# Kernel optimization log

Hardware: AMD Instinct MI355X
Metric: run time of the kernel (lower is better)

The kernel has to match this reference:

```python
import jax, jax.numpy as jnp
import numpy as np

ALPHAS = (0.1, 0.3, 0.6)
WEIGHTS = (0.5, 0.3, 0.2)
HUBER_MARGIN = 1.0
B, S = 2048, 8192


def setup_inputs() -> dict:
    key = jax.random.key(0)
    k1, k2 = jax.random.split(key)
    pred = jax.random.normal(k1, (B, S), dtype=jnp.float32)
    target = jax.random.normal(k2, (B, S), dtype=jnp.float32)
    return {"pred": pred, "target": target}


def _ema(x, alpha):
    # x: [B, S]; ema[0] = x[0]; ema[i] = alpha*x[i] + (1-alpha)*ema[i-1]
    x0 = x[:, 0]
    def step(carry, xi):
        nc = alpha * xi + (1.0 - alpha) * carry
        return nc, nc
    _, ys = jax.lax.scan(step, x0, x[:, 1:].T)  # ys: [S-1, B]
    return jnp.concatenate([x0[:, None], ys.T], axis=1)  # [B, S]


def _huber_loss(pred_delta, target_delta):
    dir_agreement = pred_delta * target_delta
    step_err = jnp.abs(pred_delta - target_delta)
    quad = jnp.square(jnp.maximum(HUBER_MARGIN - dir_agreement, 0.0)) / (2.0 * HUBER_MARGIN)
    return jnp.where(dir_agreement < 0, step_err, quad).mean(axis=1)  # [B]


def reference(pred, target):
    loss = jnp.zeros((pred.shape[0],), dtype=pred.dtype)
    for alpha, weight in zip(ALPHAS, WEIGHTS):
        pe = _ema(pred, alpha)
        te = _ema(target, alpha)
        pd = pe[:, 1:] - pe[:, :-1]
        td = te[:, 1:] - te[:, :-1]
        loss = loss + weight * _huber_loss(pd, td)
    return loss.mean()  # reduction='mean'
```

## Files before the change

### kernel.cpp

```cpp
#include <hip/hip_runtime.h>

#define B_ROWS 2048
#define S_LEN 8192
#define PER_LANE 32
#define TILE_ELEMS (64 * PER_LANE)
#define NTILES (S_LEN / TILE_ELEMS)
#define WPB 4
#define NBLOCKS (B_ROWS / WPB)

constexpr double cpowi(double b, int e) { double r = 1.0; for (int i = 0; i < e; ++i) r *= b; return r; }
constexpr float tof(double x) { return (x < 1.2e-38 && x > -1.2e-38) ? 0.0f : (float)x; }

#define A0f 0.1f
#define A1f 0.3f
#define A2f 0.6f

constexpr float D0_1 = tof(cpowi(0.9, 32)),  D0_2 = tof(cpowi(0.9, 64)),  D0_4 = tof(cpowi(0.9, 128));
constexpr float D0_8 = tof(cpowi(0.9, 256)), D0_16 = tof(cpowi(0.9, 512)), D0_32 = tof(cpowi(0.9, 1024));
constexpr float D1_1 = tof(cpowi(0.7, 32)),  D1_2 = tof(cpowi(0.7, 64)),  D1_4 = tof(cpowi(0.7, 128));
constexpr float D1_8 = tof(cpowi(0.7, 256)), D1_16 = tof(cpowi(0.7, 512)), D1_32 = tof(cpowi(0.7, 1024));
constexpr float D2_1 = tof(cpowi(0.4, 32)),  D2_2 = tof(cpowi(0.4, 64)),  D2_4 = tof(cpowi(0.4, 128));
constexpr float D2_8 = tof(cpowi(0.4, 256)), D2_16 = tof(cpowi(0.4, 512)), D2_32 = tof(cpowi(0.4, 1024));

__device__ __forceinline__ float ema_scan(float v, int lane,
                                          float d1, float d2, float d4,
                                          float d8, float d16, float d32) {
    float u;
    u = __shfl_up(v, 1);  v += (lane >= 1  ? d1  : 0.0f) * u;
    u = __shfl_up(v, 2);  v += (lane >= 2  ? d2  : 0.0f) * u;
    u = __shfl_up(v, 4);  v += (lane >= 4  ? d4  : 0.0f) * u;
    u = __shfl_up(v, 8);  v += (lane >= 8  ? d8  : 0.0f) * u;
    u = __shfl_up(v, 16); v += (lane >= 16 ? d16 : 0.0f) * u;
    u = __shfl_up(v, 32); v += (lane >= 32 ? d32 : 0.0f) * u;
    return v;
}

__device__ __forceinline__ float huber(float pd, float td) {
    float dir = pd * td;
    float se  = fabsf(pd - td);
    float mm  = fmaxf(1.0f - dir, 0.0f);
    float q   = 0.5f * mm * mm;
    return dir < 0.0f ? se : q;
}

__global__ void __launch_bounds__(256) msl_main(const float* __restrict__ pred,
                                                const float* __restrict__ targ,
                                                float* __restrict__ partial) {
    const int lane = threadIdx.x & 63;
    const int wave = threadIdx.x >> 6;
    const int row  = blockIdx.x * WPB + wave;
    const float* __restrict__ prow = pred + (size_t)row * S_LEN;
    const float* __restrict__ trow = targ + (size_t)row * S_LEN;

    float sp0 = 0.f, sp1 = 0.f, sp2 = 0.f, st0 = 0.f, st1 = 0.f, st2 = 0.f;
    float acc0 = 0.f, acc1 = 0.f, acc2 = 0.f;

    for (int tile = 0; tile < NTILES; ++tile) {
        const int base = tile * TILE_ELEMS + lane * PER_LANE;
        float xp[PER_LANE], xt[PER_LANE];
        const float4* p4 = reinterpret_cast<const float4*>(prow + base);
        const float4* t4 = reinterpret_cast<const float4*>(trow + base);
#pragma unroll
        for (int j = 0; j < PER_LANE / 4; ++j) {
            float4 a = p4[j];
            float4 b = t4[j];
            xp[4 * j + 0] = a.x; xp[4 * j + 1] = a.y; xp[4 * j + 2] = a.z; xp[4 * j + 3] = a.w;
            xt[4 * j + 0] = b.x; xt[4 * j + 1] = b.y; xt[4 * j + 2] = b.z; xt[4 * j + 3] = b.w;
        }

        const bool first = (tile == 0);
        const bool lz    = (lane == 0);

        float Lp0 = lz ? (first ? xp[0] : sp0) : 0.0f;
        float Lp1 = lz ? (first ? xp[0] : sp1) : 0.0f;
        float Lp2 = lz ? (first ? xp[0] : sp2) : 0.0f;
        float Lt0 = lz ? (first ? xt[0] : st0) : 0.0f;
        float Lt1 = lz ? (first ? xt[0] : st1) : 0.0f;
        float Lt2 = lz ? (first ? xt[0] : st2) : 0.0f;
#pragma unroll
        for (int j = 0; j < PER_LANE; ++j) {
            Lp0 += A0f * (xp[j] - Lp0);
            Lp1 += A1f * (xp[j] - Lp1);
            Lp2 += A2f * (xp[j] - Lp2);
            Lt0 += A0f * (xt[j] - Lt0);
            Lt1 += A1f * (xt[j] - Lt1);
            Lt2 += A2f * (xt[j] - Lt2);
        }

        float vp0 = ema_scan(Lp0, lane, D0_1, D0_2, D0_4, D0_8, D0_16, D0_32);
        float vp1 = ema_scan(Lp1, lane, D1_1, D1_2, D1_4, D1_8, D1_16, D1_32);
        float vp2 = ema_scan(Lp2, lane, D2_1, D2_2, D2_4, D2_8, D2_16, D2_32);
        float vt0 = ema_scan(Lt0, lane, D0_1, D0_2, D0_4, D0_8, D0_16, D0_32);
        float vt1 = ema_scan(Lt1, lane, D1_1, D1_2, D1_4, D1_8, D1_16, D1_32);
        float vt2 = ema_scan(Lt2, lane, D2_1, D2_2, D2_4, D2_8, D2_16, D2_32);

        float cp0 = __shfl_up(vp0, 1), cp1 = __shfl_up(vp1, 1), cp2 = __shfl_up(vp2, 1);
        float ct0 = __shfl_up(vt0, 1), ct1 = __shfl_up(vt1, 1), ct2 = __shfl_up(vt2, 1);

        float yp0 = lz ? (first ? xp[0] : sp0) : cp0;
        float yp1 = lz ? (first ? xp[0] : sp1) : cp1;
        float yp2 = lz ? (first ? xp[0] : sp2) : cp2;
        float yt0 = lz ? (first ? xt[0] : st0) : ct0;
        float yt1 = lz ? (first ? xt[0] : st1) : ct1;
        float yt2 = lz ? (first ? xt[0] : st2) : ct2;

        sp0 = __shfl(vp0, 63); sp1 = __shfl(vp1, 63); sp2 = __shfl(vp2, 63);
        st0 = __shfl(vt0, 63); st1 = __shfl(vt1, 63); st2 = __shfl(vt2, 63);

        const float skip = (first && lz) ? 0.0f : 1.0f;
#pragma unroll
        for (int j = 0; j < PER_LANE; ++j) {
            float pd0 = A0f * (xp[j] - yp0); yp0 += pd0;
            float td0 = A0f * (xt[j] - yt0); yt0 += td0;
            float pd1 = A1f * (xp[j] - yp1); yp1 += pd1;
            float td1 = A1f * (xt[j] - yt1); yt1 += td1;
            float pd2 = A2f * (xp[j] - yp2); yp2 += pd2;
            float td2 = A2f * (xt[j] - yt2); yt2 += td2;

            float h0 = huber(pd0, td0);
            float h1 = huber(pd1, td1);
            float h2 = huber(pd2, td2);
            if (j == 0) { h0 *= skip; h1 *= skip; h2 *= skip; }
            acc0 += h0; acc1 += h1; acc2 += h2;
        }
    }

    float wacc = 0.5f * acc0 + 0.3f * acc1 + 0.2f * acc2;
#pragma unroll
    for (int o = 32; o > 0; o >>= 1) wacc += __shfl_down(wacc, o);

    __shared__ float sred[WPB];
    if (lane == 0) sred[wave] = wacc;
    __syncthreads();
    if (threadIdx.x == 0)
        partial[blockIdx.x] = sred[0] + sred[1] + sred[2] + sred[3];
}

__global__ void __launch_bounds__(256) msl_reduce(const float* __restrict__ partial,
                                                  float* __restrict__ out) {
    const int tid = threadIdx.x;
    float v = partial[tid] + partial[tid + 256];
#pragma unroll
    for (int o = 32; o > 0; o >>= 1) v += __shfl_down(v, o);
    __shared__ float s[4];
    if ((tid & 63) == 0) s[tid >> 6] = v;
    __syncthreads();
    if (tid == 0)
        out[0] = (s[0] + s[1] + s[2] + s[3]) *
                 (float)(1.0 / ((double)(S_LEN - 1) * (double)B_ROWS));
}

extern "C" void kernel_launch(void* const* d_in, const int* in_sizes, int n_in,
                              void* d_out, int out_size, void* d_ws, size_t ws_size,
                              hipStream_t stream) {
    const float* pred = (const float*)d_in[0];
    const float* targ = (const float*)d_in[1];
    float* out = (float*)d_out;
    float* partial = (float*)d_ws;

    msl_main<<<NBLOCKS, 256, 0, stream>>>(pred, targ, partial);
    msl_reduce<<<1, 256, 0, stream>>>(partial, out);
}
```

Before: 157.4 us.

## Split rows into warm-started segments and replace reduce kernel with atomics

Each row is split into 8 segments of 1024 outputs, each handled by its own wave, which recomputes a 256-element warm-up window so the EMA state decays enough to be ignored. This gives 8x more waves and removes the serial tile loop per row. The second reduction kernel is replaced by a memset and a per-block atomicAdd. The warm-up truncation is an approximation: with alpha 0.1 the state decays by 0.9^256 (about 2e-12), which is below float precision. It costs about 25% extra loads and compute, and the atomic sum makes the result order nondeterministic.

```diff
diff --git a/kernel.cpp b/kernel.cpp
--- a/kernel.cpp
+++ b/kernel.cpp
@@ -2,36 +2,38 @@
 
 #define B_ROWS 2048
 #define S_LEN 8192
-#define PER_LANE 32
-#define TILE_ELEMS (64 * PER_LANE)
-#define NTILES (S_LEN / TILE_ELEMS)
+#define SEG_OUT 1024
+#define WARM 256
+#define EXT (SEG_OUT + WARM)
+#define PER_LANE (EXT / 64)
+#define NSEG (S_LEN / SEG_OUT)
 #define WPB 4
-#define NBLOCKS (B_ROWS / WPB)
+#define NBLOCKS (B_ROWS * NSEG / WPB)
 
 constexpr double cpowi(double b, int e) { double r = 1.0; for (int i = 0; i < e; ++i) r *= b; return r; }
-constexpr float tof(double x) { return (x < 1.2e-38 && x > -1.2e-38) ? 0.0f : (float)x; }
+constexpr float trim(double x) { return (x < 1e-12 && x > -1e-12) ? 0.0f : (float)x; }
 
 #define A0f 0.1f
 #define A1f 0.3f
 #define A2f 0.6f
 
-constexpr float D0_1 = tof(cpowi(0.9, 32)),  D0_2 = tof(cpowi(0.9, 64)),  D0_4 = tof(cpowi(0.9, 128));
-constexpr float D0_8 = tof(cpowi(0.9, 256)), D0_16 = tof(cpowi(0.9, 512)), D0_32 = tof(cpowi(0.9, 1024));
-constexpr float D1_1 = tof(cpowi(0.7, 32)),  D1_2 = tof(cpowi(0.7, 64)),  D1_4 = tof(cpowi(0.7, 128));
-constexpr float D1_8 = tof(cpowi(0.7, 256)), D1_16 = tof(cpowi(0.7, 512)), D1_32 = tof(cpowi(0.7, 1024));
-constexpr float D2_1 = tof(cpowi(0.4, 32)),  D2_2 = tof(cpowi(0.4, 64)),  D2_4 = tof(cpowi(0.4, 128));
-constexpr float D2_8 = tof(cpowi(0.4, 256)), D2_16 = tof(cpowi(0.4, 512)), D2_32 = tof(cpowi(0.4, 1024));
+constexpr float D0_1 = trim(cpowi(0.9, 20)),  D0_2 = trim(cpowi(0.9, 40)),  D0_4 = trim(cpowi(0.9, 80));
+constexpr float D0_8 = trim(cpowi(0.9, 160)), D0_16 = trim(cpowi(0.9, 320)), D0_32 = trim(cpowi(0.9, 640));
+constexpr float D1_1 = trim(cpowi(0.7, 20)),  D1_2 = trim(cpowi(0.7, 40)),  D1_4 = trim(cpowi(0.7, 80));
+constexpr float D1_8 = trim(cpowi(0.7, 160)), D1_16 = trim(cpowi(0.7, 320)), D1_32 = trim(cpowi(0.7, 640));
+constexpr float D2_1 = trim(cpowi(0.4, 20)),  D2_2 = trim(cpowi(0.4, 40)),  D2_4 = trim(cpowi(0.4, 80));
+constexpr float D2_8 = trim(cpowi(0.4, 160)), D2_16 = trim(cpowi(0.4, 320)), D2_32 = trim(cpowi(0.4, 640));
 
 __device__ __forceinline__ float ema_scan(float v, int lane,
                                           float d1, float d2, float d4,
                                           float d8, float d16, float d32) {
     float u;
-    u = __shfl_up(v, 1);  v += (lane >= 1  ? d1  : 0.0f) * u;
-    u = __shfl_up(v, 2);  v += (lane >= 2  ? d2  : 0.0f) * u;
-    u = __shfl_up(v, 4);  v += (lane >= 4  ? d4  : 0.0f) * u;
-    u = __shfl_up(v, 8);  v += (lane >= 8  ? d8  : 0.0f) * u;
-    u = __shfl_up(v, 16); v += (lane >= 16 ? d16 : 0.0f) * u;
-    u = __shfl_up(v, 32); v += (lane >= 32 ? d32 : 0.0f) * u;
+    if (d1 != 0.0f) { u = __shfl_up(v, 1);  v += (lane >= 1  ? d1  : 0.0f) * u; }
+    if (d2 != 0.0f) { u = __shfl_up(v, 2);  v += (lane >= 2  ? d2  : 0.0f) * u; }
+    if (d4 != 0.0f) { u = __shfl_up(v, 4);  v += (lane >= 4  ? d4  : 0.0f) * u; }
+    if (d8 != 0.0f) { u = __shfl_up(v, 8);  v += (lane >= 8  ? d8  : 0.0f) * u; }
+    if (d16 != 0.0f) { u = __shfl_up(v, 16); v += (lane >= 16 ? d16 : 0.0f) * u; }
+    if (d32 != 0.0f) { u = __shfl_up(v, 32); v += (lane >= 32 ? d32 : 0.0f) * u; }
     return v;
 }
 
@@ -45,84 +47,80 @@
 
 __global__ void __launch_bounds__(256) msl_main(const float* __restrict__ pred,
                                                 const float* __restrict__ targ,
-                                                float* __restrict__ partial) {
+                                                float* __restrict__ out) {
     const int lane = threadIdx.x & 63;
     const int wave = threadIdx.x >> 6;
-    const int row  = blockIdx.x * WPB + wave;
-    const float* __restrict__ prow = pred + (size_t)row * S_LEN;
-    const float* __restrict__ trow = targ + (size_t)row * S_LEN;
+    const int g    = blockIdx.x * WPB + wave;
+    const int row  = g >> 3;
+    const int seg  = g & 7;
+    const bool s0  = (seg == 0);
+    const bool lz  = (lane == 0);
 
-    float sp0 = 0.f, sp1 = 0.f, sp2 = 0.f, st0 = 0.f, st1 = 0.f, st2 = 0.f;
+    const int ext_base = s0 ? 0 : seg * SEG_OUT - WARM;
+    const int lo = s0 ? 1 : WARM;
+    const int hi = s0 ? SEG_OUT : EXT;
+
+    const float* __restrict__ prow = pred + (size_t)row * S_LEN + ext_base + lane * PER_LANE;
+    const float* __restrict__ trow = targ + (size_t)row * S_LEN + ext_base + lane * PER_LANE;
+
+    float xp[PER_LANE], xt[PER_LANE];
+    const float4* p4 = reinterpret_cast<const float4*>(prow);
+    const float4* t4 = reinterpret_cast<const float4*>(trow);
+#pragma unroll
+    for (int j = 0; j < PER_LANE / 4; ++j) {
+        float4 a = p4[j];
+        float4 b = t4[j];
+        xp[4 * j + 0] = a.x; xp[4 * j + 1] = a.y; xp[4 * j + 2] = a.z; xp[4 * j + 3] = a.w;
+        xt[4 * j + 0] = b.x; xt[4 * j + 1] = b.y; xt[4 * j + 2] = b.z; xt[4 * j + 3] = b.w;
+    }
+
+    const float ip = (lz && s0) ? xp[0] : 0.0f;
+    const float it = (lz && s0) ? xt[0] : 0.0f;
+    float Lp0 = ip, Lp1 = ip, Lp2 = ip;
+    float Lt0 = it, Lt1 = it, Lt2 = it;
+#pragma unroll
+    for (int j = 0; j < PER_LANE; ++j) {
+        Lp0 += A0f * (xp[j] - Lp0);
+        Lp1 += A1f * (xp[j] - Lp1);
+        Lp2 += A2f * (xp[j] - Lp2);
+        Lt0 += A0f * (xt[j] - Lt0);
+        Lt1 += A1f * (xt[j] - Lt1);
+        Lt2 += A2f * (xt[j] - Lt2);
+    }
+
+    float vp0 = ema_scan(Lp0, lane, D0_1, D0_2, D0_4, D0_8, D0_16, D0_32);
+    float vp1 = ema_scan(Lp1, lane, D1_1, D1_2, D1_4, D1_8, D1_16, D1_32);
+    float vp2 = ema_scan(Lp2, lane, D2_1, D2_2, D2_4, D2_8, D2_16, D2_32);
+    float vt0 = ema_scan(Lt0, lane, D0_1, D0_2, D0_4, D0_8, D0_16, D0_32);
+    float vt1 = ema_scan(Lt1, lane, D1_1, D1_2, D1_4, D1_8, D1_16, D1_32);
+    float vt2 = ema_scan(Lt2, lane, D2_1, D2_2, D2_4, D2_8, D2_16, D2_32);
+
+    float cp0 = __shfl_up(vp0, 1), cp1 = __shfl_up(vp1, 1), cp2 = __shfl_up(vp2, 1);
+    float ct0 = __shfl_up(vt0, 1), ct1 = __shfl_up(vt1, 1), ct2 = __shfl_up(vt2, 1);
+
+    float yp0 = lz ? ip : cp0;
+    float yp1 = lz ? ip : cp1;
+    float yp2 = lz ? ip : cp2;
+    float yt0 = lz ? it : ct0;
+    float yt1 = lz ? it : ct1;
+    float yt2 = lz ? it : ct2;
+
     float acc0 = 0.f, acc1 = 0.f, acc2 = 0.f;
+    const int ebase = lane * PER_LANE;
+#pragma unroll
+    for (int j = 0; j < PER_LANE; ++j) {
+        float pd0 = A0f * (xp[j] - yp0); yp0 += pd0;
+        float td0 = A0f * (xt[j] - yt0); yt0 += td0;
+        float pd1 = A1f * (xp[j] - yp1); yp1 += pd1;
+        float td1 = A1f * (xt[j] - yt1); yt1 += td1;
+        float pd2 = A2f * (xp[j] - yp2); yp2 += pd2;
+        float td2 = A2f * (xt[j] - yt2); yt2 += td2;
 
-    for (int tile = 0; tile < NTILES; ++tile) {
-        const int base = tile * TILE_ELEMS + lane * PER_LANE;
-        float xp[PER_LANE], xt[PER_LANE];
-        const float4* p4 = reinterpret_cast<const float4*>(prow + base);
-        const float4* t4 = reinterpret_cast<const float4*>(trow + base);
-#pragma unroll
-        for (int j = 0; j < PER_LANE / 4; ++j) {
-            float4 a = p4[j];
-            float4 b = t4[j];
-            xp[4 * j + 0] = a.x; xp[4 * j + 1] = a.y; xp[4 * j + 2] = a.z; xp[4 * j + 3] = a.w;
-            xt[4 * j + 0] = b.x; xt[4 * j + 1] = b.y; xt[4 * j + 2] = b.z; xt[4 * j + 3] = b.w;
-        }
-
-        const bool first = (tile == 0);
-        const bool lz    = (lane == 0);
-
-        float Lp0 = lz ? (first ? xp[0] : sp0) : 0.0f;
-        float Lp1 = lz ? (first ? xp[0] : sp1) : 0.0f;
-        float Lp2 = lz ? (first ? xp[0] : sp2) : 0.0f;
-        float Lt0 = lz ? (first ? xt[0] : st0) : 0.0f;
-        float Lt1 = lz ? (first ? xt[0] : st1) : 0.0f;
-        float Lt2 = lz ? (first ? xt[0] : st2) : 0.0f;
-#pragma unroll
-        for (int j = 0; j < PER_LANE; ++j) {
-            Lp0 += A0f * (xp[j] - Lp0);
-            Lp1 += A1f * (xp[j] - Lp1);
-            Lp2 += A2f * (xp[j] - Lp2);
-            Lt0 += A0f * (xt[j] - Lt0);
-            Lt1 += A1f * (xt[j] - Lt1);
-            Lt2 += A2f * (xt[j] - Lt2);
-        }
-
-        float vp0 = ema_scan(Lp0, lane, D0_1, D0_2, D0_4, D0_8, D0_16, D0_32);
-        float vp1 = ema_scan(Lp1, lane, D1_1, D1_2, D1_4, D1_8, D1_16, D1_32);
-        float vp2 = ema_scan(Lp2, lane, D2_1, D2_2, D2_4, D2_8, D2_16, D2_32);
-        float vt0 = ema_scan(Lt0, lane, D0_1, D0_2, D0_4, D0_8, D0_16, D0_32);
-        float vt1 = ema_scan(Lt1, lane, D1_1, D1_2, D1_4, D1_8, D1_16, D1_32);
-        float vt2 = ema_scan(Lt2, lane, D2_1, D2_2, D2_4, D2_8, D2_16, D2_32);
-
-        float cp0 = __shfl_up(vp0, 1), cp1 = __shfl_up(vp1, 1), cp2 = __shfl_up(vp2, 1);
-        float ct0 = __shfl_up(vt0, 1), ct1 = __shfl_up(vt1, 1), ct2 = __shfl_up(vt2, 1);
-
-        float yp0 = lz ? (first ? xp[0] : sp0) : cp0;
-        float yp1 = lz ? (first ? xp[0] : sp1) : cp1;
-        float yp2 = lz ? (first ? xp[0] : sp2) : cp2;
-        float yt0 = lz ? (first ? xt[0] : st0) : ct0;
-        float yt1 = lz ? (first ? xt[0] : st1) : ct1;
-        float yt2 = lz ? (first ? xt[0] : st2) : ct2;
-
-        sp0 = __shfl(vp0, 63); sp1 = __shfl(vp1, 63); sp2 = __shfl(vp2, 63);
-        st0 = __shfl(vt0, 63); st1 = __shfl(vt1, 63); st2 = __shfl(vt2, 63);
-
-        const float skip = (first && lz) ? 0.0f : 1.0f;
-#pragma unroll
-        for (int j = 0; j < PER_LANE; ++j) {
-            float pd0 = A0f * (xp[j] - yp0); yp0 += pd0;
-            float td0 = A0f * (xt[j] - yt0); yt0 += td0;
-            float pd1 = A1f * (xp[j] - yp1); yp1 += pd1;
-            float td1 = A1f * (xt[j] - yt1); yt1 += td1;
-            float pd2 = A2f * (xp[j] - yp2); yp2 += pd2;
-            float td2 = A2f * (xt[j] - yt2); yt2 += td2;
-
-            float h0 = huber(pd0, td0);
-            float h1 = huber(pd1, td1);
-            float h2 = huber(pd2, td2);
-            if (j == 0) { h0 *= skip; h1 *= skip; h2 *= skip; }
-            acc0 += h0; acc1 += h1; acc2 += h2;
-        }
+        const int e = ebase + j;
+        const float m = (e >= lo && e < hi) ? 1.0f : 0.0f;
+        acc0 += m * huber(pd0, td0);
+        acc1 += m * huber(pd1, td1);
+        acc2 += m * huber(pd2, td2);
     }
 
     float wacc = 0.5f * acc0 + 0.3f * acc1 + 0.2f * acc2;
@@ -130,24 +128,12 @@
     for (int o = 32; o > 0; o >>= 1) wacc += __shfl_down(wacc, o);
 
     __shared__ float sred[WPB];
-    if (lane == 0) sred[wave] = wacc;
+    if (lz) sred[wave] = wacc;
     __syncthreads();
-    if (threadIdx.x == 0)
-        partial[blockIdx.x] = sred[0] + sred[1] + sred[2] + sred[3];
-}
-
-__global__ void __launch_bounds__(256) msl_reduce(const float* __restrict__ partial,
-                                                  float* __restrict__ out) {
-    const int tid = threadIdx.x;
-    float v = partial[tid] + partial[tid + 256];
-#pragma unroll
-    for (int o = 32; o > 0; o >>= 1) v += __shfl_down(v, o);
-    __shared__ float s[4];
-    if ((tid & 63) == 0) s[tid >> 6] = v;
-    __syncthreads();
-    if (tid == 0)
-        out[0] = (s[0] + s[1] + s[2] + s[3]) *
-                 (float)(1.0 / ((double)(S_LEN - 1) * (double)B_ROWS));
+    if (threadIdx.x == 0) {
+        const float scale = (float)(1.0 / ((double)(S_LEN - 1) * (double)B_ROWS));
+        atomicAdd(out, (sred[0] + sred[1] + sred[2] + sred[3]) * scale);
+    }
 }
 
 extern "C" void kernel_launch(void* const* d_in, const int* in_sizes, int n_in,
@@ -156,8 +142,7 @@
     const float* pred = (const float*)d_in[0];
     const float* targ = (const float*)d_in[1];
     float* out = (float*)d_out;
-    float* partial = (float*)d_ws;
 
-    msl_main<<<NBLOCKS, 256, 0, stream>>>(pred, targ, partial);
-    msl_reduce<<<1, 256, 0, stream>>>(partial, out);
+    hipMemsetAsync(out, 0, sizeof(float), stream);
+    msl_main<<<NBLOCKS, 256, 0, stream>>>(pred, targ, out);
 }
```

Result: slower. 174.2 us (+10.6%).
